# Performance work log

Hardware: AMD Instinct MI355X
Metric: run time of the kernel (lower is better)

## Reference

```python
import jax, jax.numpy as jnp
import numpy as np

N_WIRES = 6
DIM = 1 << N_WIRES  # 64, equals input channel dim C for amplitude encoding
HID = N_WIRES       # hidden_dim = len(ops)


def _rx(theta):
    c = jnp.cos(theta / 2).astype(jnp.complex64)
    s = jnp.sin(theta / 2).astype(jnp.complex64)
    return jnp.stack([jnp.stack([c, -1j * s]), jnp.stack([-1j * s, c])])


def _ry(theta):
    c = jnp.cos(theta / 2).astype(jnp.complex64)
    s = jnp.sin(theta / 2).astype(jnp.complex64)
    return jnp.stack([jnp.stack([c, -s]), jnp.stack([s, c])])


def _apply_1q(state, U, wire):
    # state: (N, 2, 2, ..., 2); apply 2x2 U on qubit axis wire+1
    s = jnp.moveaxis(state, wire + 1, 1)
    s = jnp.einsum('ab,nb...->na...', U, s)
    return jnp.moveaxis(s, 1, wire + 1)


def _apply_cnot(state, c, t):
    # flip target axis where control bit == 1
    s = jnp.moveaxis(state, (c + 1, t + 1), (1, 2))
    s = jnp.concatenate([s[:, :1], jnp.flip(s[:, 1:2], axis=2)], axis=1)
    return jnp.moveaxis(s, (1, 2), (c + 1, t + 1))


def _expval_z(state, wire):
    # <Z_wire> = P(bit=0) - P(bit=1)
    p = state.real ** 2 + state.imag ** 2
    p = jnp.moveaxis(p, wire + 1, 1).reshape(p.shape[0], 2, -1)
    return p[:, 0].sum(-1) - p[:, 1].sum(-1)


def _value_layer(x_flat, params, qk):
    # amplitude encoding: normalize input into state amplitudes (C == DIM)
    norm = jnp.linalg.norm(x_flat, axis=-1, keepdims=True)
    psi = (x_flat / norm).astype(jnp.complex64)
    state = psi.reshape((x_flat.shape[0],) + (2,) * N_WIRES)
    rx0, ry0, ry1 = params[0], params[1], params[2]
    for j in range(N_WIRES):
        state = _apply_1q(state, _rx(rx0[j]), j)
        state = _apply_1q(state, _ry(ry0[j]), j)
    for j in range(N_WIRES):
        state = _apply_cnot(state, j, (j + 1) % N_WIRES)
    for j in range(N_WIRES):
        state = _apply_1q(state, _ry(ry1[j]), j)
    if qk:
        z0 = _expval_z(state, 0)
        return jnp.stack([z0] * HID, axis=-1)  # qk=True replicates wire-0 <Z>
    return jnp.stack([_expval_z(state, w) for w in range(N_WIRES)], axis=-1)


def setup_inputs() -> dict:
    key = jax.random.key(0)
    k1, k2, k3, k4 = jax.random.split(key, 4)
    B, T, C = 16, 2048, DIM
    return {
        'x': jax.random.normal(k1, (B, T, C), dtype=jnp.float32),
        'params_q': jax.random.normal(k2, (3, N_WIRES), dtype=jnp.float32),
        'params_k': jax.random.normal(k3, (3, N_WIRES), dtype=jnp.float32),
        'params_v': jax.random.normal(k4, (3, N_WIRES), dtype=jnp.float32),
    }


def reference(x, params_q, params_k, params_v):
    B, T, C = x.shape
    xf = x.reshape(B * T, C)
    q = _value_layer(xf, params_q, True).reshape(B, T, HID)
    k = _value_layer(xf, params_k, True).reshape(B, T, HID)
    v = _value_layer(xf, params_v, False).reshape(B, T, HID)
    scores = jnp.einsum('btd,bsd->bts', q, k) / jnp.sqrt(jnp.float32(HID))
    attn = jax.nn.softmax(scores, axis=-1)
    return jnp.einsum('bts,bsd->btd', attn, v)
```

## Files before the change

kernel.cpp:

```cpp
#include <hip/hip_runtime.h>
#include <math.h>

#define NWIRES 6
#define DIM 64
#define NTOK 32768
#define NBATCH 16
#define TPB 2048
#define NMOM 16
#define SQRT6F 2.4494897427831781f
#define APAD 76
#define ZP 260

typedef short bf16x8 __attribute__((ext_vector_type(8)));
typedef float f32x4  __attribute__((ext_vector_type(4)));

__device__ __forceinline__ unsigned f2bfbits(float f) {
    unsigned u = __float_as_uint(f);
    return (u + 0x7FFF + ((u >> 16) & 1)) >> 16;
}
__device__ __forceinline__ float bfbits2f(unsigned b) {
    return __uint_as_float(b << 16);
}
__device__ __forceinline__ float pswap(float v) { return __shfl_xor(v, 1, 64); }


__device__ __forceinline__ void build_A(const float* __restrict__ p,
        unsigned short* sAh, unsigned short* sAl,
        float* sTc, float* sTs, float* sP, int tid) {
    if (tid < 64) {
        int b = tid;
        float d = 0.f;
#pragma unroll
        for (int j = 0; j < 6; ++j)
            d += 0.5f * p[j] * ((b & (32 >> j)) ? -1.f : 1.f);
        float sd, cd;
        sincosf(d, &sd, &cd);
        sTc[b] = cd;
        sTs[b] = sd;
        if (b < 12) {
            float s, cc;
            sincosf(0.5f * p[6 + b], &s, &cc);
            sP[b * 2 + 0] = cc;
            sP[b * 2 + 1] = s;
        }
    }
    __syncthreads();

    {
        int ph = tid >> 7;
        int k  = (tid >> 1) & 63;
        int h  = tid & 1;
        const float* sTx = ph ? sTs : sTc;
        float v[32];
#pragma unroll
        for (int i = 0; i < 32; ++i) {
            int g = h * 32 + i;
            v[i] = (__popc(g & k) & 1) ? -sTx[g] : sTx[g];
        }
#pragma unroll
        for (int i = 0; i < 32; ++i) {
            float pv_ = pswap(v[i]);
            v[i] = h ? (pv_ - v[i]) : (v[i] + pv_);
        }
#pragma unroll
        for (int M = 16; M >= 1; M >>= 1) {
#pragma unroll
            for (int i = 0; i < 32; ++i) {
                if (i & M) continue;
                int j = i | M;
                float a = v[i], b = v[j];
                v[i] = a + b; v[j] = a - b;
            }
        }
#pragma unroll
        for (int layer = 0; layer < 2; ++layer) {
            const float* Pl = sP + layer * 12;
            {
                float c = Pl[0], ss = h ? Pl[1] : -Pl[1];
#pragma unroll
                for (int i = 0; i < 32; ++i) {
                    float pv_ = pswap(v[i]);
                    v[i] = c * v[i] + ss * pv_;
                }
            }
#pragma unroll
            for (int w = 1; w < 6; ++w) {
                int M = 32 >> w;
                float c = Pl[w * 2], s = Pl[w * 2 + 1];
#pragma unroll
                for (int i = 0; i < 32; ++i) {
                    if (i & M) continue;
                    int j = i | M;
                    float a = v[i], b = v[j];
                    v[i] = c * a - s * b;
                    v[j] = s * a + c * b;
                }
            }
            if (layer == 0) {
#pragma unroll
                for (int i = 0; i < 16; ++i) {
                    int j = i | 16;
                    float a = v[i], b = v[j];
                    v[i] = h ? b : a;
                    v[j] = h ? a : b;
                }
#pragma unroll
                for (int w = 1; w < 5; ++w) {
                    int MC = 32 >> w, MT = MC >> 1;
#pragma unroll
                    for (int i = 0; i < 32; ++i) {
                        if (!(i & MC) || (i & MT)) continue;
                        int j = i | MT;
                        float t = v[i]; v[i] = v[j]; v[j] = t;
                    }
                }
#pragma unroll
                for (int i = 1; i < 32; i += 2) v[i] = pswap(v[i]);
            }
        }
#pragma unroll
        for (int i = 0; i < 32; ++i) {
            int row = ph * 64 + h * 32 + i;
            unsigned hb = f2bfbits(v[i]);
            unsigned lb = f2bfbits(v[i] - bfbits2f(hb));
            sAh[row * APAD + k] = (unsigned short)hb;
            sAl[row * APAD + k] = (unsigned short)lb;
        }
    }
    __syncthreads();
}

__global__ __attribute__((amdgpu_waves_per_eu(1, 4)))
__launch_bounds__(256) void qsa_sim(
        const float* __restrict__ x,
        const float* __restrict__ pq,
        const float* __restrict__ pk,
        const float* __restrict__ pv,
        float* __restrict__ zq,
        float* __restrict__ mpart) {
    __shared__ __align__(16) unsigned short sAbuf[4 * 128 * APAD];
    __shared__ float sTc[64], sTs[64], sP[24];
    __shared__ float zT[256];
    __shared__ __align__(16) float vT[6 * ZP];
    __shared__ float sred[224];
    int tid = threadIdx.x;
    int tbase = blockIdx.x * 256;
    int circ = blockIdx.y;

    int lane = tid & 63, wv = tid >> 6;
    int q4 = lane >> 4, c16 = lane & 15;
    float4 rw[8];
#pragma unroll
    for (int cg = 0; cg < 2; ++cg) {
        const float* xr = x + ((size_t)(tbase + wv * 64 + cg * 16 + c16)) * 64;
#pragma unroll
        for (int ks = 0; ks < 2; ++ks) {
            rw[cg * 4 + ks * 2 + 0] = *(const float4*)(xr + ks * 32 + q4 * 8);
            rw[cg * 4 + ks * 2 + 1] = *(const float4*)(xr + ks * 32 + q4 * 8 + 4);
        }
    }

    int ncirc;
    if (circ == 0) {
        build_A(pq, sAbuf, sAbuf + 128 * APAD, sTc, sTs, sP, tid);
        ncirc = 1;
    } else {
        build_A(pk, sAbuf, sAbuf + 128 * APAD, sTc, sTs, sP, tid);
        build_A(pv, sAbuf + 2 * 128 * APAD, sAbuf + 3 * 128 * APAD,
                sTc, sTs, sP, tid);
        ncirc = 2;
    }

    bf16x8 xh[2][2], xl[2][2];
#pragma unroll 1
    for (int pr = 0; pr < 2; ++pr) {
#pragma unroll
        for (int cg = 0; cg < 2; ++cg) {
#pragma unroll
            for (int ks = 0; ks < 2; ++ks) {
                float4 f0 = rw[cg * 4 + ks * 2], f1 = rw[cg * 4 + ks * 2 + 1];
                float ff[8] = {f0.x, f0.y, f0.z, f0.w, f1.x, f1.y, f1.z, f1.w};
#pragma unroll
                for (int e = 0; e < 8; ++e) {
                    unsigned hb = f2bfbits(ff[e]);
                    unsigned lb = f2bfbits(ff[e] - bfbits2f(hb));
                    xh[cg][ks][e] = (short)hb;
                    xl[cg][ks][e] = (short)lb;
                }
            }
        }
        if (pr == 0) {
#pragma unroll
            for (int cg = 0; cg < 2; ++cg) {
                const float* xr = x + ((size_t)(tbase + wv * 64 + (2 + cg) * 16 + c16)) * 64;
#pragma unroll
                for (int ks = 0; ks < 2; ++ks) {
                    rw[cg * 4 + ks * 2 + 0] = *(const float4*)(xr + ks * 32 + q4 * 8);
                    rw[cg * 4 + ks * 2 + 1] = *(const float4*)(xr + ks * 32 + q4 * 8 + 4);
                }
            }
        }

#pragma unroll 1
        for (int cc = 0; cc < ncirc; ++cc) {
            const unsigned short* Ah = sAbuf + cc * (2 * 128 * APAD);
            const unsigned short* Al = Ah + 128 * APAD;

            f32x4 acc[2][8];
#pragma unroll
            for (int cg = 0; cg < 2; ++cg)
#pragma unroll
                for (int mt = 0; mt < 8; ++mt) acc[cg][mt] = (f32x4){0.f, 0.f, 0.f, 0.f};

#pragma unroll
            for (int mt = 0; mt < 8; ++mt) {
                int r = mt * 16 + c16;
#pragma unroll
                for (int ks = 0; ks < 2; ++ks) {
                    const uint2* ph_ = (const uint2*)(&Ah[r * APAD + ks * 32 + q4 * 8]);
                    const uint2* pl_ = (const uint2*)(&Al[r * APAD + ks * 32 + q4 * 8]);
                    union { uint2 u[2]; bf16x8 v; } ua, ub;
                    ua.u[0] = ph_[0]; ua.u[1] = ph_[1];
                    ub.u[0] = pl_[0]; ub.u[1] = pl_[1];
                    bf16x8 ah = ua.v, al = ub.v;
#pragma unroll
                    for (int cg = 0; cg < 2; ++cg) {
                        acc[cg][mt] = __builtin_amdgcn_mfma_f32_16x16x32_bf16(ah, xh[cg][ks], acc[cg][mt], 0, 0, 0);
                        acc[cg][mt] = __builtin_amdgcn_mfma_f32_16x16x32_bf16(ah, xl[cg][ks], acc[cg][mt], 0, 0, 0);
                        acc[cg][mt] = __builtin_amdgcn_mfma_f32_16x16x32_bf16(al, xh[cg][ks], acc[cg][mt], 0, 0, 0);
                    }
                }
            }

#pragma unroll
            for (int cg = 0; cg < 2; ++cg) {
                float n = 0.f, s0 = 0.f, s1 = 0.f, s2 = 0.f, s3 = 0.f, s4 = 0.f, s5 = 0.f;
                float f2 = (q4 < 2) ? 1.f : 0.f;
                float f3 = (q4 & 1) ? 0.f : 1.f;
#pragma unroll
                for (int mt = 0; mt < 4; ++mt) {
#pragma unroll
                    for (int rg = 0; rg < 4; ++rg) {
                        float dc = acc[cg][mt][rg];
                        float ds = acc[cg][mt + 4][rg];
                        float pp = dc * dc + ds * ds;
                        n += pp;
                        if (!(mt & 2)) s0 += pp;
                        if (!(mt & 1)) s1 += pp;
                        s2 += f2 * pp;
                        s3 += f3 * pp;
                        if (!(rg & 2)) s4 += pp;
                        if (!(rg & 1)) s5 += pp;
                    }
                }
#pragma unroll
                for (int d = 16; d <= 32; d <<= 1) {
                    n  += __shfl_xor(n,  d, 64);
                    s0 += __shfl_xor(s0, d, 64);
                    s1 += __shfl_xor(s1, d, 64);
                    s2 += __shfl_xor(s2, d, 64);
                    s3 += __shfl_xor(s3, d, 64);
                    s4 += __shfl_xor(s4, d, 64);
                    s5 += __shfl_xor(s5, d, 64);
                }
                if (q4 == 0) {
                    int tl = wv * 64 + (pr * 2 + cg) * 16 + c16;
                    float inv = 1.0f / n;
                    if (circ == 0) {
                        zq[tbase + tl] = SQRT6F * (2.f * s0 - n) * inv;
                    } else if (cc == 0) {
                        zT[tl] = (2.f * s0 - n) * inv;
                    } else {
                        vT[0 * ZP + tl] = (2.f * s0 - n) * inv;
                        vT[1 * ZP + tl] = (2.f * s1 - n) * inv;
                        vT[2 * ZP + tl] = (2.f * s2 - n) * inv;
                        vT[3 * ZP + tl] = (2.f * s3 - n) * inv;
                        vT[4 * ZP + tl] = (2.f * s4 - n) * inv;
                        vT[5 * ZP + tl] = (2.f * s5 - n) * inv;
                    }
                }
            }
        }
    }

    if (circ == 1) {
        __syncthreads();
        float* zpow = (float*)sAbuf;
        {
            float z = zT[tid];
            float pw = 1.f;
#pragma unroll
            for (int m = 0; m < NMOM; ++m) { zpow[m * ZP + tid] = pw; pw *= z; }
        }
        __syncthreads();
        if (tid < 224) {
            int h = (tid >= 112) ? 1 : 0;
            int j = tid - h * 112;
            int m = j / 7, w = j - m * 7;
            const float4* zp = (const float4*)&zpow[m * ZP + h * 128];
            float a = 0.f;
            if (w == 6) {
#pragma unroll
                for (int k = 0; k < 32; ++k) {
                    float4 a4 = zp[k];
                    a += a4.x + a4.y + a4.z + a4.w;
                }
            } else {
                const float4* vp = (const float4*)&vT[w * ZP + h * 128];
#pragma unroll
                for (int k = 0; k < 32; ++k) {
                    float4 a4 = zp[k], b4 = vp[k];
                    a += a4.x * b4.x + a4.y * b4.y + a4.z * b4.z + a4.w * b4.w;
                }
            }
            sred[tid] = a;
        }
        __syncthreads();
        if (tid < 112) {
            int m = tid / 7, w = tid - m * 7;
            int idx = m * 7 + ((w == 6) ? 0 : (w + 1));
            mpart[(size_t)blockIdx.x * 112 + idx] = sred[tid] + sred[tid + 112];
        }
    }
}

__global__ __launch_bounds__(256) void qsa_eval(
        const float* __restrict__ zq,
        const float* __restrict__ mpart,
        float* __restrict__ out) {
    __shared__ float sm[112];
    int bk = blockIdx.x;
    int b = bk >> 3;
    int tid = threadIdx.x;
    if (tid < 112) {
        float s = 0.f;
#pragma unroll
        for (int c = 0; c < 8; ++c) s += mpart[(size_t)(b * 8 + c) * 112 + tid];
        sm[tid] = s;
    }
    __syncthreads();

    int t = bk * 256 + tid;
    float a = zq[t];
    float den = 0.f, o0 = 0.f, o1 = 0.f, o2 = 0.f, o3 = 0.f, o4 = 0.f, o5 = 0.f;
    float pw = 1.f;
#pragma unroll
    for (int m = 0; m < NMOM; ++m) {
        const float* mm = sm + m * 7;
        den += pw * mm[0];
        o0 += pw * mm[1]; o1 += pw * mm[2]; o2 += pw * mm[3];
        o3 += pw * mm[4]; o4 += pw * mm[5]; o5 += pw * mm[6];
        pw *= a * (1.0f / (m + 1));
    }
    float inv = 1.0f / den;
    float* o = out + (size_t)t * 6;
    float2* o2p = (float2*)o;
    o2p[0] = make_float2(o0 * inv, o1 * inv);
    o2p[1] = make_float2(o2 * inv, o3 * inv);
    o2p[2] = make_float2(o4 * inv, o5 * inv);
}

extern "C" void kernel_launch(void* const* d_in, const int* in_sizes, int n_in,
                              void* d_out, int out_size, void* d_ws, size_t ws_size,
                              hipStream_t stream) {
    const float* x  = (const float*)d_in[0];
    const float* pq = (const float*)d_in[1];
    const float* pk = (const float*)d_in[2];
    const float* pv = (const float*)d_in[3];
    float* w = (float*)d_ws;
    float* zq    = w;
    float* mpart = zq + NTOK;
    float* out   = (float*)d_out;

    qsa_sim<<<dim3(NTOK / 256, 2), 256, 0, stream>>>(x, pq, pk, pv, zq, mpart);
    qsa_eval<<<NTOK / 256, 256, 0, stream>>>(zq, mpart, out);
}
```

Measured before the change: 85.07 us.

## Fuse q/k/v circuits into one block per 128 tokens

```diff
diff --git a/kernel.cpp b/kernel.cpp
--- a/kernel.cpp
+++ b/kernel.cpp
@@ -9,7 +9,7 @@
 #define NMOM 16
 #define SQRT6F 2.4494897427831781f
 #define APAD 76
-#define ZP 260
+#define ZPH 132
 
 typedef short bf16x8 __attribute__((ext_vector_type(8)));
 typedef float f32x4  __attribute__((ext_vector_type(4)));
@@ -138,21 +138,21 @@
         const float* __restrict__ pv,
         float* __restrict__ zq,
         float* __restrict__ mpart) {
-    __shared__ __align__(16) unsigned short sAbuf[4 * 128 * APAD];
+    __shared__ __align__(16) unsigned short sAbuf[6 * 128 * APAD];
     __shared__ float sTc[64], sTs[64], sP[24];
-    __shared__ float zT[256];
-    __shared__ __align__(16) float vT[6 * ZP];
+    __shared__ float zT[128];
+    __shared__ __align__(16) float vT[6 * ZPH];
     __shared__ float sred[224];
     int tid = threadIdx.x;
-    int tbase = blockIdx.x * 256;
-    int circ = blockIdx.y;
+    int bx = blockIdx.x;
+    int tbase = bx * 128;
 
     int lane = tid & 63, wv = tid >> 6;
     int q4 = lane >> 4, c16 = lane & 15;
     float4 rw[8];
 #pragma unroll
     for (int cg = 0; cg < 2; ++cg) {
-        const float* xr = x + ((size_t)(tbase + wv * 64 + cg * 16 + c16)) * 64;
+        const float* xr = x + ((size_t)(tbase + wv * 32 + cg * 16 + c16)) * 64;
 #pragma unroll
         for (int ks = 0; ks < 2; ++ks) {
             rw[cg * 4 + ks * 2 + 0] = *(const float4*)(xr + ks * 32 + q4 * 8);
@@ -160,167 +160,144 @@
         }
     }
 
-    int ncirc;
-    if (circ == 0) {
-        build_A(pq, sAbuf, sAbuf + 128 * APAD, sTc, sTs, sP, tid);
-        ncirc = 1;
-    } else {
-        build_A(pk, sAbuf, sAbuf + 128 * APAD, sTc, sTs, sP, tid);
-        build_A(pv, sAbuf + 2 * 128 * APAD, sAbuf + 3 * 128 * APAD,
-                sTc, sTs, sP, tid);
-        ncirc = 2;
-    }
+    build_A(pq, sAbuf + 0 * 128 * APAD, sAbuf + 1 * 128 * APAD, sTc, sTs, sP, tid);
+    build_A(pk, sAbuf + 2 * 128 * APAD, sAbuf + 3 * 128 * APAD, sTc, sTs, sP, tid);
+    build_A(pv, sAbuf + 4 * 128 * APAD, sAbuf + 5 * 128 * APAD, sTc, sTs, sP, tid);
 
     bf16x8 xh[2][2], xl[2][2];
+#pragma unroll
+    for (int cg = 0; cg < 2; ++cg) {
+#pragma unroll
+        for (int ks = 0; ks < 2; ++ks) {
+            float4 f0 = rw[cg * 4 + ks * 2], f1 = rw[cg * 4 + ks * 2 + 1];
+            float ff[8] = {f0.x, f0.y, f0.z, f0.w, f1.x, f1.y, f1.z, f1.w};
+#pragma unroll
+            for (int e = 0; e < 8; ++e) {
+                unsigned hb = f2bfbits(ff[e]);
+                unsigned lb = f2bfbits(ff[e] - bfbits2f(hb));
+                xh[cg][ks][e] = (short)hb;
+                xl[cg][ks][e] = (short)lb;
+            }
+        }
+    }
+
 #pragma unroll 1
-    for (int pr = 0; pr < 2; ++pr) {
+    for (int cc = 0; cc < 3; ++cc) {
+        const unsigned short* Ah = sAbuf + cc * (2 * 128 * APAD);
+        const unsigned short* Al = Ah + 128 * APAD;
+
+        f32x4 acc[2][8];
+#pragma unroll
+        for (int cg = 0; cg < 2; ++cg)
+#pragma unroll
+            for (int mt = 0; mt < 8; ++mt) acc[cg][mt] = (f32x4){0.f, 0.f, 0.f, 0.f};
+
+#pragma unroll
+        for (int mt = 0; mt < 8; ++mt) {
+            int r = mt * 16 + c16;
+#pragma unroll
+            for (int ks = 0; ks < 2; ++ks) {
+                const uint2* ph_ = (const uint2*)(&Ah[r * APAD + ks * 32 + q4 * 8]);
+                const uint2* pl_ = (const uint2*)(&Al[r * APAD + ks * 32 + q4 * 8]);
+                union { uint2 u[2]; bf16x8 v; } ua, ub;
+                ua.u[0] = ph_[0]; ua.u[1] = ph_[1];
+                ub.u[0] = pl_[0]; ub.u[1] = pl_[1];
+                bf16x8 ah = ua.v, al = ub.v;
+#pragma unroll
+                for (int cg = 0; cg < 2; ++cg) {
+                    acc[cg][mt] = __builtin_amdgcn_mfma_f32_16x16x32_bf16(ah, xh[cg][ks], acc[cg][mt], 0, 0, 0);
+                    acc[cg][mt] = __builtin_amdgcn_mfma_f32_16x16x32_bf16(ah, xl[cg][ks], acc[cg][mt], 0, 0, 0);
+                    acc[cg][mt] = __builtin_amdgcn_mfma_f32_16x16x32_bf16(al, xh[cg][ks], acc[cg][mt], 0, 0, 0);
+                }
+            }
+        }
+
 #pragma unroll
         for (int cg = 0; cg < 2; ++cg) {
-#pragma unroll
-            for (int ks = 0; ks < 2; ++ks) {
-                float4 f0 = rw[cg * 4 + ks * 2], f1 = rw[cg * 4 + ks * 2 + 1];
-                float ff[8] = {f0.x, f0.y, f0.z, f0.w, f1.x, f1.y, f1.z, f1.w};
-#pragma unroll
-                for (int e = 0; e < 8; ++e) {
-                    unsigned hb = f2bfbits(ff[e]);
-                    unsigned lb = f2bfbits(ff[e] - bfbits2f(hb));
-                    xh[cg][ks][e] = (short)hb;
-                    xl[cg][ks][e] = (short)lb;
-                }
-            }
-        }
-        if (pr == 0) {
-#pragma unroll
-            for (int cg = 0; cg < 2; ++cg) {
-                const float* xr = x + ((size_t)(tbase + wv * 64 + (2 + cg) * 16 + c16)) * 64;
-#pragma unroll
-                for (int ks = 0; ks < 2; ++ks) {
-                    rw[cg * 4 + ks * 2 + 0] = *(const float4*)(xr + ks * 32 + q4 * 8);
-                    rw[cg * 4 + ks * 2 + 1] = *(const float4*)(xr + ks * 32 + q4 * 8 + 4);
-                }
-            }
-        }
-
-#pragma unroll 1
-        for (int cc = 0; cc < ncirc; ++cc) {
-            const unsigned short* Ah = sAbuf + cc * (2 * 128 * APAD);
-            const unsigned short* Al = Ah + 128 * APAD;
-
-            f32x4 acc[2][8];
-#pragma unroll
-            for (int cg = 0; cg < 2; ++cg)
-#pragma unroll
-                for (int mt = 0; mt < 8; ++mt) acc[cg][mt] = (f32x4){0.f, 0.f, 0.f, 0.f};
-
-#pragma unroll
-            for (int mt = 0; mt < 8; ++mt) {
-                int r = mt * 16 + c16;
-#pragma unroll
-                for (int ks = 0; ks < 2; ++ks) {
-                    const uint2* ph_ = (const uint2*)(&Ah[r * APAD + ks * 32 + q4 * 8]);
-                    const uint2* pl_ = (const uint2*)(&Al[r * APAD + ks * 32 + q4 * 8]);
-                    union { uint2 u[2]; bf16x8 v; } ua, ub;
-                    ua.u[0] = ph_[0]; ua.u[1] = ph_[1];
-                    ub.u[0] = pl_[0]; ub.u[1] = pl_[1];
-                    bf16x8 ah = ua.v, al = ub.v;
-#pragma unroll
-                    for (int cg = 0; cg < 2; ++cg) {
-                        acc[cg][mt] = __builtin_amdgcn_mfma_f32_16x16x32_bf16(ah, xh[cg][ks], acc[cg][mt], 0, 0, 0);
-                        acc[cg][mt] = __builtin_amdgcn_mfma_f32_16x16x32_bf16(ah, xl[cg][ks], acc[cg][mt], 0, 0, 0);
-                        acc[cg][mt] = __builtin_amdgcn_mfma_f32_16x16x32_bf16(al, xh[cg][ks], acc[cg][mt], 0, 0, 0);
-                    }
-                }
-            }
-
-#pragma unroll
-            for (int cg = 0; cg < 2; ++cg) {
-                float n = 0.f, s0 = 0.f, s1 = 0.f, s2 = 0.f, s3 = 0.f, s4 = 0.f, s5 = 0.f;
-                float f2 = (q4 < 2) ? 1.f : 0.f;
-                float f3 = (q4 & 1) ? 0.f : 1.f;
-#pragma unroll
-                for (int mt = 0; mt < 4; ++mt) {
-#pragma unroll
-                    for (int rg = 0; rg < 4; ++rg) {
-                        float dc = acc[cg][mt][rg];
-                        float ds = acc[cg][mt + 4][rg];
-                        float pp = dc * dc + ds * ds;
-                        n += pp;
-                        if (!(mt & 2)) s0 += pp;
-                        if (!(mt & 1)) s1 += pp;
-                        s2 += f2 * pp;
-                        s3 += f3 * pp;
-                        if (!(rg & 2)) s4 += pp;
-                        if (!(rg & 1)) s5 += pp;
-                    }
-                }
-#pragma unroll
-                for (int d = 16; d <= 32; d <<= 1) {
-                    n  += __shfl_xor(n,  d, 64);
-                    s0 += __shfl_xor(s0, d, 64);
-                    s1 += __shfl_xor(s1, d, 64);
-                    s2 += __shfl_xor(s2, d, 64);
-                    s3 += __shfl_xor(s3, d, 64);
-                    s4 += __shfl_xor(s4, d, 64);
-                    s5 += __shfl_xor(s5, d, 64);
-                }
-                if (q4 == 0) {
-                    int tl = wv * 64 + (pr * 2 + cg) * 16 + c16;
-                    float inv = 1.0f / n;
-                    if (circ == 0) {
-                        zq[tbase + tl] = SQRT6F * (2.f * s0 - n) * inv;
-                    } else if (cc == 0) {
-                        zT[tl] = (2.f * s0 - n) * inv;
-                    } else {
-                        vT[0 * ZP + tl] = (2.f * s0 - n) * inv;
-                        vT[1 * ZP + tl] = (2.f * s1 - n) * inv;
-                        vT[2 * ZP + tl] = (2.f * s2 - n) * inv;
-                        vT[3 * ZP + tl] = (2.f * s3 - n) * inv;
-                        vT[4 * ZP + tl] = (2.f * s4 - n) * inv;
-                        vT[5 * ZP + tl] = (2.f * s5 - n) * inv;
-                    }
-                }
-            }
-        }
-    }
-
-    if (circ == 1) {
-        __syncthreads();
-        float* zpow = (float*)sAbuf;
-        {
-            float z = zT[tid];
-            float pw = 1.f;
-#pragma unroll
-            for (int m = 0; m < NMOM; ++m) { zpow[m * ZP + tid] = pw; pw *= z; }
-        }
-        __syncthreads();
-        if (tid < 224) {
-            int h = (tid >= 112) ? 1 : 0;
-            int j = tid - h * 112;
-            int m = j / 7, w = j - m * 7;
-            const float4* zp = (const float4*)&zpow[m * ZP + h * 128];
-            float a = 0.f;
-            if (w == 6) {
-#pragma unroll
-                for (int k = 0; k < 32; ++k) {
-                    float4 a4 = zp[k];
-                    a += a4.x + a4.y + a4.z + a4.w;
-                }
-            } else {
-                const float4* vp = (const float4*)&vT[w * ZP + h * 128];
-#pragma unroll
-                for (int k = 0; k < 32; ++k) {
-                    float4 a4 = zp[k], b4 = vp[k];
-                    a += a4.x * b4.x + a4.y * b4.y + a4.z * b4.z + a4.w * b4.w;
-                }
-            }
-            sred[tid] = a;
-        }
-        __syncthreads();
-        if (tid < 112) {
-            int m = tid / 7, w = tid - m * 7;
-            int idx = m * 7 + ((w == 6) ? 0 : (w + 1));
-            mpart[(size_t)blockIdx.x * 112 + idx] = sred[tid] + sred[tid + 112];
-        }
+            float n = 0.f, s0 = 0.f, s1 = 0.f, s2 = 0.f, s3 = 0.f, s4 = 0.f, s5 = 0.f;
+            float f2 = (q4 < 2) ? 1.f : 0.f;
+            float f3 = (q4 & 1) ? 0.f : 1.f;
+#pragma unroll
+            for (int mt = 0; mt < 4; ++mt) {
+#pragma unroll
+                for (int rg = 0; rg < 4; ++rg) {
+                    float dc = acc[cg][mt][rg];
+                    float ds = acc[cg][mt + 4][rg];
+                    float pp = dc * dc + ds * ds;
+                    n += pp;
+                    if (!(mt & 2)) s0 += pp;
+                    if (!(mt & 1)) s1 += pp;
+                    s2 += f2 * pp;
+                    s3 += f3 * pp;
+                    if (!(rg & 2)) s4 += pp;
+                    if (!(rg & 1)) s5 += pp;
+                }
+            }
+#pragma unroll
+            for (int d = 16; d <= 32; d <<= 1) {
+                n  += __shfl_xor(n,  d, 64);
+                s0 += __shfl_xor(s0, d, 64);
+                s1 += __shfl_xor(s1, d, 64);
+                s2 += __shfl_xor(s2, d, 64);
+                s3 += __shfl_xor(s3, d, 64);
+                s4 += __shfl_xor(s4, d, 64);
+                s5 += __shfl_xor(s5, d, 64);
+            }
+            if (q4 == 0) {
+                int tl = wv * 32 + cg * 16 + c16;
+                float inv = 1.0f / n;
+                if (cc == 0) {
+                    zq[tbase + tl] = SQRT6F * (2.f * s0 - n) * inv;
+                } else if (cc == 1) {
+                    zT[tl] = (2.f * s0 - n) * inv;
+                } else {
+                    vT[0 * ZPH + tl] = (2.f * s0 - n) * inv;
+                    vT[1 * ZPH + tl] = (2.f * s1 - n) * inv;
+                    vT[2 * ZPH + tl] = (2.f * s2 - n) * inv;
+                    vT[3 * ZPH + tl] = (2.f * s3 - n) * inv;
+                    vT[4 * ZPH + tl] = (2.f * s4 - n) * inv;
+                    vT[5 * ZPH + tl] = (2.f * s5 - n) * inv;
+                }
+            }
+        }
+    }
+
+    __syncthreads();
+    float* zpow = (float*)sAbuf;
+    if (tid < 128) {
+        float z = zT[tid];
+        float pw = 1.f;
+#pragma unroll
+        for (int m = 0; m < NMOM; ++m) { zpow[m * ZPH + tid] = pw; pw *= z; }
+    }
+    __syncthreads();
+    if (tid < 224) {
+        int h = (tid >= 112) ? 1 : 0;
+        int j = tid - h * 112;
+        int m = j / 7, w = j - m * 7;
+        const float4* zp = (const float4*)&zpow[m * ZPH + h * 64];
+        float a = 0.f;
+        if (w == 6) {
+#pragma unroll
+            for (int k = 0; k < 16; ++k) {
+                float4 a4 = zp[k];
+                a += a4.x + a4.y + a4.z + a4.w;
+            }
+        } else {
+            const float4* vp = (const float4*)&vT[w * ZPH + h * 64];
+#pragma unroll
+            for (int k = 0; k < 16; ++k) {
+                float4 a4 = zp[k], b4 = vp[k];
+                a += a4.x * b4.x + a4.y * b4.y + a4.z * b4.z + a4.w * b4.w;
+            }
+        }
+        sred[tid] = a;
+    }
+    __syncthreads();
+    if (tid < 112) {
+        int m = tid / 7, w = tid - m * 7;
+        int idx = m * 7 + ((w == 6) ? 0 : (w + 1));
+        mpart[(size_t)bx * 112 + idx] = sred[tid] + sred[tid + 112];
     }
 }
 
@@ -335,7 +312,7 @@
     if (tid < 112) {
         float s = 0.f;
 #pragma unroll
-        for (int c = 0; c < 8; ++c) s += mpart[(size_t)(b * 8 + c) * 112 + tid];
+        for (int c = 0; c < 16; ++c) s += mpart[(size_t)(b * 16 + c) * 112 + tid];
         sm[tid] = s;
     }
     __syncthreads();
@@ -372,6 +349,6 @@
     float* mpart = zq + NTOK;
     float* out   = (float*)d_out;
 
-    qsa_sim<<<dim3(NTOK / 256, 2), 256, 0, stream>>>(x, pq, pk, pv, zq, mpart);
+    qsa_sim<<<256, 256, 0, stream>>>(x, pq, pk, pv, zq, mpart);
     qsa_eval<<<NTOK / 256, 256, 0, stream>>>(zq, mpart, out);
 }
```

Measured after the change: 86.69 us. Within noise of the previous version (+1.9%).
